# Optimization experiments

Measured on AMD Instinct MI355X. Metric: run time of the kernel, lower is better.

The kernel has to match this reference:

```python
import jax, jax.numpy as jnp
import numpy as np

B, A, T, D, H, K, P = 32, 32, 64, 16, 64, 2, 2
E = A * (A - 1)
TAU = 0.5


def _linear_init(key, fin, fout):
    bound = 1.0 / np.sqrt(fin)
    kw, kb = jax.random.split(key)
    W = jax.random.uniform(kw, (fin, fout), minval=-bound, maxval=bound, dtype=jnp.float32)
    b = jax.random.uniform(kb, (fout,), minval=-bound, maxval=bound, dtype=jnp.float32)
    return W, b


def setup_inputs() -> dict:
    key = jax.random.key(0)
    ks = jax.random.split(key, 12)
    # off-diagonal edge list; rel_rec/rel_send are one-hot [E, A]
    idx = np.array([(i, j) for i in range(A) for j in range(A) if i != j])
    eye = np.eye(A, dtype=np.float32)
    rel_rec = jnp.asarray(eye[idx[:, 0]])
    rel_send = jnp.asarray(eye[idx[:, 1]])
    inputs = jax.random.normal(ks[0], (B, A, T, D), dtype=jnp.float32)
    rel_graph = 0.1 * jax.random.normal(ks[1], (1, 1, E, K), dtype=jnp.float32)
    u = jax.random.uniform(ks[2], (1, 1, E, K), minval=1e-6, maxval=1.0 - 1e-6)
    gumbel = -jnp.log(-jnp.log(u))
    # per-edge-type message MLPs, stacked over K
    w1, b1, w2, b2 = [], [], [], []
    for k in range(K):
        Wa, ba = _linear_init(jax.random.fold_in(ks[3], k), 2 * D, H)
        Wb, bb = _linear_init(jax.random.fold_in(ks[4], k), H, H)
        w1.append(Wa); b1.append(ba); w2.append(Wb); b2.append(bb)
    msg_W1 = jnp.stack(w1); msg_b1 = jnp.stack(b1)
    msg_W2 = jnp.stack(w2); msg_b2 = jnp.stack(b2)
    out_W1, out_b1 = _linear_init(ks[5], D + H, H)
    out_W2, out_b2 = _linear_init(ks[6], H, H)
    out_W3, out_b3 = _linear_init(ks[7], H, D)
    return {"inputs": inputs, "rel_rec": rel_rec, "rel_send": rel_send,
            "rel_graph": rel_graph, "gumbel": gumbel,
            "msg_W1": msg_W1, "msg_b1": msg_b1, "msg_W2": msg_W2, "msg_b2": msg_b2,
            "out_W1": out_W1, "out_b1": out_b1, "out_W2": out_W2, "out_b2": out_b2,
            "out_W3": out_W3, "out_b3": out_b3}


def _single_step(xs, edges, rel_rec, rel_send,
                 msg_W1, msg_b1, msg_W2, msg_b2,
                 out_W1, out_b1, out_W2, out_b2, out_W3, out_b3):
    # xs: [B, Ts, A, D]; gather endpoints -> [B, Ts, E, D]
    recv = jnp.einsum('ea,btad->bted', rel_rec, xs)
    send = jnp.einsum('ea,btad->bted', rel_send, xs)
    pre_msg = jnp.concatenate([send, recv], axis=-1)  # [B,Ts,E,2D]
    all_msgs = jnp.zeros(pre_msg.shape[:-1] + (H,), dtype=xs.dtype)
    for k in range(K):  # small fixed loop over edge types
        m = jax.nn.relu(pre_msg @ msg_W1[k] + msg_b1[k])
        m = jax.nn.relu(m @ msg_W2[k] + msg_b2[k])
        all_msgs = all_msgs + m * edges[..., k:k + 1]
    # scatter-sum messages to receiver nodes: [B,Ts,A,H]
    agg = jnp.einsum('bteh,ea->btah', all_msgs, rel_rec)
    aug = jnp.concatenate([xs, agg], axis=-1)
    p = jax.nn.relu(aug @ out_W1 + out_b1)
    p = jax.nn.relu(p @ out_W2 + out_b2)
    p = p @ out_W3 + out_b3
    return xs + p


def reference(inputs, rel_rec, rel_send, rel_graph, gumbel,
              msg_W1, msg_b1, msg_W2, msg_b2,
              out_W1, out_b1, out_W2, out_b2, out_W3, out_b3):
    # soft gumbel-softmax (hard=False, deterministic via provided noise)
    edges = jax.nn.softmax((rel_graph + gumbel) / TAU, axis=-1)  # [1,1,E,K]
    x = jnp.transpose(inputs, (0, 2, 1, 3))  # [B,T,A,D]
    last = x[:, ::P]  # [B, T/P, A, D]
    preds = []
    for _ in range(P):
        last = _single_step(last, edges, rel_rec, rel_send,
                            msg_W1, msg_b1, msg_W2, msg_b2,
                            out_W1, out_b1, out_W2, out_b2, out_W3, out_b3)
        preds.append(last)
    # interleave: output[:, t*P + i] = preds[i][:, t]
    out = jnp.stack(preds, axis=2).reshape(x.shape[0], -1, A, D)[:, :T - 1]
    return jnp.transpose(out, (0, 2, 1, 3))  # [B, A, T-1, D]
```

## Files before the change

### kernel.cpp

```cpp
#include <hip/hip_runtime.h>

typedef unsigned short u16;
typedef unsigned int u32;
typedef __attribute__((ext_vector_type(8))) short bf16x8;
typedef __attribute__((ext_vector_type(4))) float f32x4;
typedef __attribute__((ext_vector_type(4))) u32 u32x4;

__device__ __forceinline__ u32 cvtpk(float lo, float hi) {
    u32 r; asm("v_cvt_pk_bf16_f32 %0, %1, %2" : "=v"(r) : "v"(lo), "v"(hi)); return r;
}
__device__ __forceinline__ u16 f2bf1(float f) { return (u16)(cvtpk(f, f) & 0xffffu); }

__device__ __forceinline__ u16 f2bf(float f) {
    union { float f; unsigned u; } v; v.f = f;
    unsigned r = (v.u + 0x7FFFu + ((v.u >> 16) & 1u)) >> 16;
    return (u16)r;
}

__global__ void edge_softmax_k(const float* __restrict__ rg,
                               const float* __restrict__ gb,
                               float* __restrict__ ew) {
    int tid = blockIdx.x * 256 + threadIdx.x;
    if (tid >= 1024) return;
    int i = tid >> 5, j = tid & 31;
    float w0 = 0.f, w1 = 0.f;
    if (i != j) {
        int e = i * 31 + j - (j > i ? 1 : 0);
        float a0 = (rg[e * 2 + 0] + gb[e * 2 + 0]) * 2.0f;
        float a1 = (rg[e * 2 + 1] + gb[e * 2 + 1]) * 2.0f;
        float m = fmaxf(a0, a1);
        float e0 = expf(a0 - m), e1 = expf(a1 - m);
        float s = e0 + e1;
        w0 = e0 / s; w1 = e1 / s;
    }
    ew[tid * 2 + 0] = w0;
    ew[tid * 2 + 1] = w1;
}

__global__ void pack_weights_k(const float* __restrict__ W1,
                               const float* __restrict__ W2,
                               const float* __restrict__ OW1,
                               const float* __restrict__ OW2,
                               const float* __restrict__ OW3,
                               u16* __restrict__ wp) {
    int tid = blockIdx.x * 256 + threadIdx.x;
    if (tid < 4096) {
        int j = tid & 7, l = (tid >> 3) & 63, t = (tid >> 9) & 3, k = tid >> 11;
        int kk = 8 * (l >> 4) + j;
        int n  = 32 * (t >> 1) + 8 * ((l & 15) >> 2) + 4 * (t & 1) + (l & 3);
        wp[tid] = f2bf(W1[k * 2048 + kk * 64 + n]);
    } else if (tid < 12288) {
        int x = tid - 4096;
        int j = x & 7, l = (x >> 3) & 63, t = (x >> 9) & 3, s = (x >> 11) & 1, k = x >> 12;
        int kk = 32 * s + 8 * (l >> 4) + j, n = 16 * t + (l & 15);
        wp[tid] = f2bf(W2[k * 4096 + kk * 64 + n]);
    } else if (tid < 18432) {
        int x = tid - 12288;
        int j = x & 7, l = (x >> 3) & 63, t = (x >> 9) & 3, s = x >> 11;
        int kk = 32 * s + 8 * (l >> 4) + j, n = 16 * t + (l & 15);
        wp[tid] = f2bf(kk < 80 ? OW1[kk * 64 + n] : 0.f);
    } else if (tid < 22528) {
        int x = tid - 18432;
        int j = x & 7, l = (x >> 3) & 63, t = (x >> 9) & 3, s = x >> 11;
        int kk = 32 * s + 8 * (l >> 4) + j, n = 16 * t + (l & 15);
        wp[tid] = f2bf(OW2[kk * 64 + n]);
    } else if (tid < 23552) {
        int x = tid - 22528;
        int j = x & 7, l = (x >> 3) & 63, s = x >> 9;
        int kk = 32 * s + 8 * (l >> 4) + j, n = (l & 15);
        wp[tid] = f2bf(OW3[kk * 16 + n]);
    }
}

__global__ __launch_bounds__(256, 2) void nri_decoder_k(
    const float* __restrict__ inputs,
    const float* __restrict__ mb1, const float* __restrict__ mb2,
    const float* __restrict__ ob1, const float* __restrict__ ob2,
    const float* __restrict__ ob3,
    const float* __restrict__ ew,
    const u16*  __restrict__ wp,
    float* __restrict__ out)
{
    __shared__ float xsf[32][16];
    __shared__ __align__(16) u16 xsb[32][24];
    __shared__ __align__(16) float agg2[2][32][68];
    __shared__ __align__(16) u16 augb[32][104];
    __shared__ __align__(16) u16 p1b[32][72];
    __shared__ __align__(16) u16 p2b[32][72];

    const int tid = threadIdx.x;
    const int w = tid >> 6, lane = tid & 63, g = lane >> 4, lr = lane & 15;
    const int kw = w >> 1, w01 = w & 1;
    const int b = blockIdx.x >> 5, tp = blockIdx.x & 31;

    const u16* w1tp = wp;
    const u16* w2p  = wp + 4096;
    const u16* ow1p = wp + 12288;
    const u16* ow2p = wp + 18432;
    const u16* ow3p = wp + 22528;

    for (int idx = tid; idx < 512; idx += 256) {
        int a = idx >> 4, d = idx & 15;
        float v = inputs[(((b * 32 + a) * 64) + 2 * tp) * 16 + d];
        u16 bv = f2bf1(v);
        xsf[a][d] = v;
        xsb[a][d] = bv;
        augb[a][d] = bv;
        augb[a][80 + d] = 0;
    }

    bf16x8 w1t[4], w2f[2][4];
#pragma unroll
    for (int t = 0; t < 4; ++t)
        w1t[t] = *(const bf16x8*)(w1tp + ((kw * 4 + t) * 64 + lane) * 8);
#pragma unroll
    for (int s = 0; s < 2; ++s)
#pragma unroll
        for (int t = 0; t < 4; ++t)
            w2f[s][t] = *(const bf16x8*)(w2p + (((kw * 2 + s) * 4 + t) * 64 + lane) * 8);

    f32x4 b1c[4];
    float b2r[4];
#pragma unroll
    for (int t = 0; t < 4; ++t) {
#pragma unroll
        for (int r = 0; r < 4; ++r)
            b1c[t][r] = mb1[kw * 64 + 32 * (t >> 1) + 8 * g + 4 * (t & 1) + r];
        b2r[t] = mb2[kw * 64 + 16 * t + lr];
    }
    float o1r[4], o2r[4];
#pragma unroll
    for (int t = 0; t < 4; ++t) { o1r[t] = ob1[16 * t + lr]; o2r[t] = ob2[16 * t + lr]; }
    const float o3r = ob3[lr];

    __syncthreads();

    for (int step = 0; step < 2; ++step) {
        for (int p = 0; p < 16; ++p) {
            const int ir = 16 * w01 + p;
            float racc[4] = {0.f, 0.f, 0.f, 0.f};
#pragma unroll
            for (int half = 0; half < 2; ++half) {
                const int m = 2 * ir + half;
                const int e0 = m * 16;
                const int srow = (g < 2) ? (16 * (m & 1) + lr) : (m >> 1);
                const bf16x8 bfrag = *(const bf16x8*)(&xsb[srow][(g & 1) * 8]);

                float ewv[4];
#pragma unroll
                for (int r = 0; r < 4; ++r) ewv[r] = ew[(e0 + 4 * g + r) * 2 + kw];

                f32x4 c0 = __builtin_amdgcn_mfma_f32_16x16x32_bf16(w1t[0], bfrag, b1c[0], 0, 0, 0);
                f32x4 c1 = __builtin_amdgcn_mfma_f32_16x16x32_bf16(w1t[1], bfrag, b1c[1], 0, 0, 0);
                f32x4 c2 = __builtin_amdgcn_mfma_f32_16x16x32_bf16(w1t[2], bfrag, b1c[2], 0, 0, 0);
                f32x4 c3 = __builtin_amdgcn_mfma_f32_16x16x32_bf16(w1t[3], bfrag, b1c[3], 0, 0, 0);

                union { u32 u[8]; bf16x8 v[2]; } a2;
                a2.u[0] = cvtpk(fmaxf(c0[0], 0.f), fmaxf(c0[1], 0.f));
                a2.u[1] = cvtpk(fmaxf(c0[2], 0.f), fmaxf(c0[3], 0.f));
                a2.u[2] = cvtpk(fmaxf(c1[0], 0.f), fmaxf(c1[1], 0.f));
                a2.u[3] = cvtpk(fmaxf(c1[2], 0.f), fmaxf(c1[3], 0.f));
                a2.u[4] = cvtpk(fmaxf(c2[0], 0.f), fmaxf(c2[1], 0.f));
                a2.u[5] = cvtpk(fmaxf(c2[2], 0.f), fmaxf(c2[3], 0.f));
                a2.u[6] = cvtpk(fmaxf(c3[0], 0.f), fmaxf(c3[1], 0.f));
                a2.u[7] = cvtpk(fmaxf(c3[2], 0.f), fmaxf(c3[3], 0.f));

#pragma unroll
                for (int t = 0; t < 4; ++t) {
                    f32x4 d = {b2r[t], b2r[t], b2r[t], b2r[t]};
                    d = __builtin_amdgcn_mfma_f32_16x16x32_bf16(a2.v[0], w2f[0][t], d, 0, 0, 0);
                    d = __builtin_amdgcn_mfma_f32_16x16x32_bf16(a2.v[1], w2f[1][t], d, 0, 0, 0);
#pragma unroll
                    for (int r = 0; r < 4; ++r)
                        racc[t] += fmaxf(d[r], 0.f) * ewv[r];
                }
            }
#pragma unroll
            for (int t = 0; t < 4; ++t) {
                racc[t] += __shfl_xor(racc[t], 16);
                racc[t] += __shfl_xor(racc[t], 32);
            }
            float v = (g & 2) ? ((g & 1) ? racc[3] : racc[2])
                              : ((g & 1) ? racc[1] : racc[0]);
            agg2[kw][ir][16 * g + lr] = v;
        }
        __syncthreads();

        {
            const int a = tid >> 3, cc = (tid & 7) * 8;
            f32x4 x0 = *(const f32x4*)&agg2[0][a][cc];
            f32x4 x1 = *(const f32x4*)&agg2[0][a][cc + 4];
            f32x4 y0 = *(const f32x4*)&agg2[1][a][cc];
            f32x4 y1 = *(const f32x4*)&agg2[1][a][cc + 4];
            x0 += y0; x1 += y1;
            u32x4 q = { cvtpk(x0[0], x0[1]), cvtpk(x0[2], x0[3]),
                        cvtpk(x1[0], x1[1]), cvtpk(x1[2], x1[3]) };
            *(u32x4*)&augb[a][16 + cc] = q;
        }
        __syncthreads();

        {
            f32x4 c0 = {o1r[w], o1r[w], o1r[w], o1r[w]};
            f32x4 c1 = c0;
#pragma unroll
            for (int s = 0; s < 3; ++s) {
                const bf16x8 a0 = *(const bf16x8*)(&augb[lr][32 * s + 8 * g]);
                const bf16x8 a1 = *(const bf16x8*)(&augb[16 + lr][32 * s + 8 * g]);
                const bf16x8 bw = *(const bf16x8*)(ow1p + ((s * 4 + w) * 64 + lane) * 8);
                c0 = __builtin_amdgcn_mfma_f32_16x16x32_bf16(a0, bw, c0, 0, 0, 0);
                c1 = __builtin_amdgcn_mfma_f32_16x16x32_bf16(a1, bw, c1, 0, 0, 0);
            }
#pragma unroll
            for (int r = 0; r < 4; ++r) {
                p1b[4 * g + r][16 * w + lr]      = f2bf1(fmaxf(c0[r], 0.f));
                p1b[16 + 4 * g + r][16 * w + lr] = f2bf1(fmaxf(c1[r], 0.f));
            }
        }
        __syncthreads();

        {
            f32x4 c0 = {o2r[w], o2r[w], o2r[w], o2r[w]};
            f32x4 c1 = c0;
#pragma unroll
            for (int s = 0; s < 2; ++s) {
                const bf16x8 a0 = *(const bf16x8*)(&p1b[lr][32 * s + 8 * g]);
                const bf16x8 a1 = *(const bf16x8*)(&p1b[16 + lr][32 * s + 8 * g]);
                const bf16x8 bw = *(const bf16x8*)(ow2p + ((s * 4 + w) * 64 + lane) * 8);
                c0 = __builtin_amdgcn_mfma_f32_16x16x32_bf16(a0, bw, c0, 0, 0, 0);
                c1 = __builtin_amdgcn_mfma_f32_16x16x32_bf16(a1, bw, c1, 0, 0, 0);
            }
#pragma unroll
            for (int r = 0; r < 4; ++r) {
                p2b[4 * g + r][16 * w + lr]      = f2bf1(fmaxf(c0[r], 0.f));
                p2b[16 + 4 * g + r][16 * w + lr] = f2bf1(fmaxf(c1[r], 0.f));
            }
        }
        __syncthreads();

        if (w < 2) {
            f32x4 c = {o3r, o3r, o3r, o3r};
#pragma unroll
            for (int s = 0; s < 2; ++s) {
                const bf16x8 a0 = *(const bf16x8*)(&p2b[16 * w + lr][32 * s + 8 * g]);
                const bf16x8 bw = *(const bf16x8*)(ow3p + (s * 64 + lane) * 8);
                c = __builtin_amdgcn_mfma_f32_16x16x32_bf16(a0, bw, c, 0, 0, 0);
            }
            const int tt = 2 * tp + step;
#pragma unroll
            for (int r = 0; r < 4; ++r) {
                const int aa = 16 * w + 4 * g + r;
                const float nv = xsf[aa][lr] + c[r];
                u16 bv = f2bf1(nv);
                xsf[aa][lr] = nv;
                xsb[aa][lr] = bv;
                augb[aa][lr] = bv;
                if (tt < 63) out[(((b * 32 + aa) * 63) + tt) * 16 + lr] = nv;
            }
        }
        __syncthreads();
    }
}

extern "C" void kernel_launch(void* const* d_in, const int* in_sizes, int n_in,
                              void* d_out, int out_size, void* d_ws, size_t ws_size,
                              hipStream_t stream) {
    const float* inputs = (const float*)d_in[0];
    const float* rg     = (const float*)d_in[3];
    const float* gb     = (const float*)d_in[4];
    const float* W1     = (const float*)d_in[5];
    const float* mb1    = (const float*)d_in[6];
    const float* W2     = (const float*)d_in[7];
    const float* mb2    = (const float*)d_in[8];
    const float* OW1    = (const float*)d_in[9];
    const float* ob1    = (const float*)d_in[10];
    const float* OW2    = (const float*)d_in[11];
    const float* ob2    = (const float*)d_in[12];
    const float* OW3    = (const float*)d_in[13];
    const float* ob3    = (const float*)d_in[14];

    float* ew = (float*)d_ws;
    u16*   wpk = (u16*)((char*)d_ws + 8192);

    edge_softmax_k<<<4, 256, 0, stream>>>(rg, gb, ew);
    pack_weights_k<<<92, 256, 0, stream>>>(W1, W2, OW1, OW2, OW3, wpk);
    nri_decoder_k<<<1024, 256, 0, stream>>>(inputs, mb1, mb2, ob1, ob2, ob3,
                                            ew, wpk, (float*)d_out);
}
```

Before: 84.46 us.

## Fuse output MLP into register chain using transposed MFMA and LDS-staged weights

```diff
diff --git a/kernel.cpp b/kernel.cpp
--- a/kernel.cpp
+++ b/kernel.cpp
@@ -4,12 +4,12 @@
 typedef unsigned int u32;
 typedef __attribute__((ext_vector_type(8))) short bf16x8;
 typedef __attribute__((ext_vector_type(4))) float f32x4;
+typedef __attribute__((ext_vector_type(2))) u32 u32x2;
 typedef __attribute__((ext_vector_type(4))) u32 u32x4;
 
 __device__ __forceinline__ u32 cvtpk(float lo, float hi) {
     u32 r; asm("v_cvt_pk_bf16_f32 %0, %1, %2" : "=v"(r) : "v"(lo), "v"(hi)); return r;
 }
-__device__ __forceinline__ u16 f2bf1(float f) { return (u16)(cvtpk(f, f) & 0xffffu); }
 
 __device__ __forceinline__ u16 f2bf(float f) {
     union { float f; unsigned u; } v; v.f = f;
@@ -56,19 +56,23 @@
         wp[tid] = f2bf(W2[k * 4096 + kk * 64 + n]);
     } else if (tid < 18432) {
         int x = tid - 12288;
-        int j = x & 7, l = (x >> 3) & 63, t = (x >> 9) & 3, s = x >> 11;
-        int kk = 32 * s + 8 * (l >> 4) + j, n = 16 * t + (l & 15);
-        wp[tid] = f2bf(kk < 80 ? OW1[kk * 64 + n] : 0.f);
+        int j = x & 7, l = (x >> 3) & 63, ts = x >> 9;
+        int s = ts % 3, t = ts / 3;
+        int kk = 32 * s + 8 * (l >> 4) + j;
+        int feat = 32 * (t >> 1) + 8 * ((l & 15) >> 2) + 4 * (t & 1) + (l & 3);
+        wp[tid] = f2bf(kk < 80 ? OW1[kk * 64 + feat] : 0.f);
     } else if (tid < 22528) {
         int x = tid - 18432;
-        int j = x & 7, l = (x >> 3) & 63, t = (x >> 9) & 3, s = x >> 11;
-        int kk = 32 * s + 8 * (l >> 4) + j, n = 16 * t + (l & 15);
-        wp[tid] = f2bf(OW2[kk * 64 + n]);
+        int j = x & 7, l = (x >> 3) & 63, ts = x >> 9;
+        int s = ts & 1, t = ts >> 1;
+        int kk = 32 * s + 8 * (l >> 4) + j;
+        int feat = 32 * (t >> 1) + 8 * ((l & 15) >> 2) + 4 * (t & 1) + (l & 3);
+        wp[tid] = f2bf(OW2[kk * 64 + feat]);
     } else if (tid < 23552) {
         int x = tid - 22528;
         int j = x & 7, l = (x >> 3) & 63, s = x >> 9;
-        int kk = 32 * s + 8 * (l >> 4) + j, n = (l & 15);
-        wp[tid] = f2bf(OW3[kk * 16 + n]);
+        int kk = 32 * s + 8 * (l >> 4) + j;
+        wp[tid] = f2bf(OW3[kk * 16 + (l & 15)]);
     }
 }
 
@@ -81,12 +85,10 @@
     const u16*  __restrict__ wp,
     float* __restrict__ out)
 {
-    __shared__ float xsf[32][16];
-    __shared__ __align__(16) u16 xsb[32][24];
+    __shared__ __align__(16) u16 xsb[2][32][24];
     __shared__ __align__(16) float agg2[2][32][68];
-    __shared__ __align__(16) u16 augb[32][104];
-    __shared__ __align__(16) u16 p1b[32][72];
-    __shared__ __align__(16) u16 p2b[32][72];
+    __shared__ __align__(16) u16 augb[2][32][104];
+    __shared__ __align__(16) u16 owlds[11264];
 
     const int tid = threadIdx.x;
     const int w = tid >> 6, lane = tid & 63, g = lane >> 4, lr = lane & 15;
@@ -95,19 +97,19 @@
 
     const u16* w1tp = wp;
     const u16* w2p  = wp + 4096;
-    const u16* ow1p = wp + 12288;
-    const u16* ow2p = wp + 18432;
-    const u16* ow3p = wp + 22528;
-
-    for (int idx = tid; idx < 512; idx += 256) {
-        int a = idx >> 4, d = idx & 15;
-        float v = inputs[(((b * 32 + a) * 64) + 2 * tp) * 16 + d];
-        u16 bv = f2bf1(v);
-        xsf[a][d] = v;
-        xsb[a][d] = bv;
-        augb[a][d] = bv;
-        augb[a][80 + d] = 0;
-    }
+
+    for (int idx = tid; idx < 1408; idx += 256)
+        *(u32x4*)(&owlds[idx * 8]) = *(const u32x4*)(wp + 12288 + idx * 8);
+
+    if (tid < 128) {
+        const int a = tid >> 2, dd = (tid & 3) * 4;
+        const f32x4 v = *(const f32x4*)(inputs + (((b * 32 + a) * 64) + 2 * tp) * 16 + dd);
+        u32x2 q = { cvtpk(v[0], v[1]), cvtpk(v[2], v[3]) };
+        *(u32x2*)(&xsb[0][a][dd]) = q;
+        *(u32x2*)(&augb[0][a][dd]) = q;
+    }
+    for (int idx = tid; idx < 1024; idx += 256)
+        augb[idx >> 9][(idx >> 4) & 31][80 + (idx & 15)] = 0;
 
     bf16x8 w1t[4], w2f[2][4];
 #pragma unroll
@@ -119,23 +121,31 @@
         for (int t = 0; t < 4; ++t)
             w2f[s][t] = *(const bf16x8*)(w2p + (((kw * 2 + s) * 4 + t) * 64 + lane) * 8);
 
-    f32x4 b1c[4];
+    f32x4 b1c[4], o1c[4], o2c[4], o3c;
     float b2r[4];
 #pragma unroll
     for (int t = 0; t < 4; ++t) {
 #pragma unroll
-        for (int r = 0; r < 4; ++r)
-            b1c[t][r] = mb1[kw * 64 + 32 * (t >> 1) + 8 * g + 4 * (t & 1) + r];
+        for (int r = 0; r < 4; ++r) {
+            const int pi = 32 * (t >> 1) + 8 * g + 4 * (t & 1) + r;
+            b1c[t][r] = mb1[kw * 64 + pi];
+            o1c[t][r] = ob1[pi];
+            o2c[t][r] = ob2[pi];
+        }
         b2r[t] = mb2[kw * 64 + 16 * t + lr];
     }
-    float o1r[4], o2r[4];
-#pragma unroll
-    for (int t = 0; t < 4; ++t) { o1r[t] = ob1[16 * t + lr]; o2r[t] = ob2[16 * t + lr]; }
-    const float o3r = ob3[lr];
+#pragma unroll
+    for (int r = 0; r < 4; ++r) o3c[r] = ob3[4 * g + r];
+
+    const int u = w & 1;
+    const int arow = 16 * u + lr;
+    f32x4 xsreg = *(const f32x4*)(inputs + (((b * 32 + arow) * 64) + 2 * tp) * 16 + 4 * g);
 
     __syncthreads();
 
     for (int step = 0; step < 2; ++step) {
+        const int sp = step & 1;
+
         for (int p = 0; p < 16; ++p) {
             const int ir = 16 * w01 + p;
             float racc[4] = {0.f, 0.f, 0.f, 0.f};
@@ -144,7 +154,7 @@
                 const int m = 2 * ir + half;
                 const int e0 = m * 16;
                 const int srow = (g < 2) ? (16 * (m & 1) + lr) : (m >> 1);
-                const bf16x8 bfrag = *(const bf16x8*)(&xsb[srow][(g & 1) * 8]);
+                const bf16x8 bfrag = *(const bf16x8*)(&xsb[sp][srow][(g & 1) * 8]);
 
                 float ewv[4];
 #pragma unroll
@@ -155,15 +165,15 @@
                 f32x4 c2 = __builtin_amdgcn_mfma_f32_16x16x32_bf16(w1t[2], bfrag, b1c[2], 0, 0, 0);
                 f32x4 c3 = __builtin_amdgcn_mfma_f32_16x16x32_bf16(w1t[3], bfrag, b1c[3], 0, 0, 0);
 
-                union { u32 u[8]; bf16x8 v[2]; } a2;
-                a2.u[0] = cvtpk(fmaxf(c0[0], 0.f), fmaxf(c0[1], 0.f));
-                a2.u[1] = cvtpk(fmaxf(c0[2], 0.f), fmaxf(c0[3], 0.f));
-                a2.u[2] = cvtpk(fmaxf(c1[0], 0.f), fmaxf(c1[1], 0.f));
-                a2.u[3] = cvtpk(fmaxf(c1[2], 0.f), fmaxf(c1[3], 0.f));
-                a2.u[4] = cvtpk(fmaxf(c2[0], 0.f), fmaxf(c2[1], 0.f));
-                a2.u[5] = cvtpk(fmaxf(c2[2], 0.f), fmaxf(c2[3], 0.f));
-                a2.u[6] = cvtpk(fmaxf(c3[0], 0.f), fmaxf(c3[1], 0.f));
-                a2.u[7] = cvtpk(fmaxf(c3[2], 0.f), fmaxf(c3[3], 0.f));
+                union { u32 q[8]; bf16x8 v[2]; } a2;
+                a2.q[0] = cvtpk(fmaxf(c0[0], 0.f), fmaxf(c0[1], 0.f));
+                a2.q[1] = cvtpk(fmaxf(c0[2], 0.f), fmaxf(c0[3], 0.f));
+                a2.q[2] = cvtpk(fmaxf(c1[0], 0.f), fmaxf(c1[1], 0.f));
+                a2.q[3] = cvtpk(fmaxf(c1[2], 0.f), fmaxf(c1[3], 0.f));
+                a2.q[4] = cvtpk(fmaxf(c2[0], 0.f), fmaxf(c2[1], 0.f));
+                a2.q[5] = cvtpk(fmaxf(c2[2], 0.f), fmaxf(c2[3], 0.f));
+                a2.q[6] = cvtpk(fmaxf(c3[0], 0.f), fmaxf(c3[1], 0.f));
+                a2.q[7] = cvtpk(fmaxf(c3[2], 0.f), fmaxf(c3[3], 0.f));
 
 #pragma unroll
                 for (int t = 0; t < 4; ++t) {
@@ -195,66 +205,68 @@
             x0 += y0; x1 += y1;
             u32x4 q = { cvtpk(x0[0], x0[1]), cvtpk(x0[2], x0[3]),
                         cvtpk(x1[0], x1[1]), cvtpk(x1[2], x1[3]) };
-            *(u32x4*)&augb[a][16 + cc] = q;
+            *(u32x4*)&augb[sp][a][16 + cc] = q;
         }
         __syncthreads();
 
         {
-            f32x4 c0 = {o1r[w], o1r[w], o1r[w], o1r[w]};
-            f32x4 c1 = c0;
+            f32x4 c[4] = {o1c[0], o1c[1], o1c[2], o1c[3]};
 #pragma unroll
             for (int s = 0; s < 3; ++s) {
-                const bf16x8 a0 = *(const bf16x8*)(&augb[lr][32 * s + 8 * g]);
-                const bf16x8 a1 = *(const bf16x8*)(&augb[16 + lr][32 * s + 8 * g]);
-                const bf16x8 bw = *(const bf16x8*)(ow1p + ((s * 4 + w) * 64 + lane) * 8);
-                c0 = __builtin_amdgcn_mfma_f32_16x16x32_bf16(a0, bw, c0, 0, 0, 0);
-                c1 = __builtin_amdgcn_mfma_f32_16x16x32_bf16(a1, bw, c1, 0, 0, 0);
-            }
-#pragma unroll
-            for (int r = 0; r < 4; ++r) {
-                p1b[4 * g + r][16 * w + lr]      = f2bf1(fmaxf(c0[r], 0.f));
-                p1b[16 + 4 * g + r][16 * w + lr] = f2bf1(fmaxf(c1[r], 0.f));
-            }
-        }
-        __syncthreads();
-
-        {
-            f32x4 c0 = {o2r[w], o2r[w], o2r[w], o2r[w]};
-            f32x4 c1 = c0;
+                const bf16x8 bB = *(const bf16x8*)(&augb[sp][arow][32 * s + 8 * g]);
+#pragma unroll
+                for (int t = 0; t < 4; ++t) {
+                    const bf16x8 aA = *(const bf16x8*)(&owlds[(t * 3 + s) * 512 + lane * 8]);
+                    c[t] = __builtin_amdgcn_mfma_f32_16x16x32_bf16(aA, bB, c[t], 0, 0, 0);
+                }
+            }
+            union { u32 q[8]; bf16x8 v[2]; } pa;
+            pa.q[0] = cvtpk(fmaxf(c[0][0], 0.f), fmaxf(c[0][1], 0.f));
+            pa.q[1] = cvtpk(fmaxf(c[0][2], 0.f), fmaxf(c[0][3], 0.f));
+            pa.q[2] = cvtpk(fmaxf(c[1][0], 0.f), fmaxf(c[1][1], 0.f));
+            pa.q[3] = cvtpk(fmaxf(c[1][2], 0.f), fmaxf(c[1][3], 0.f));
+            pa.q[4] = cvtpk(fmaxf(c[2][0], 0.f), fmaxf(c[2][1], 0.f));
+            pa.q[5] = cvtpk(fmaxf(c[2][2], 0.f), fmaxf(c[2][3], 0.f));
+            pa.q[6] = cvtpk(fmaxf(c[3][0], 0.f), fmaxf(c[3][1], 0.f));
+            pa.q[7] = cvtpk(fmaxf(c[3][2], 0.f), fmaxf(c[3][3], 0.f));
+
+            f32x4 c2[4] = {o2c[0], o2c[1], o2c[2], o2c[3]};
+#pragma unroll
+            for (int s = 0; s < 2; ++s)
+#pragma unroll
+                for (int t = 0; t < 4; ++t) {
+                    const bf16x8 aA = *(const bf16x8*)(&owlds[6144 + (t * 2 + s) * 512 + lane * 8]);
+                    c2[t] = __builtin_amdgcn_mfma_f32_16x16x32_bf16(aA, pa.v[s], c2[t], 0, 0, 0);
+                }
+            union { u32 q[8]; bf16x8 v[2]; } pb;
+            pb.q[0] = cvtpk(fmaxf(c2[0][0], 0.f), fmaxf(c2[0][1], 0.f));
+            pb.q[1] = cvtpk(fmaxf(c2[0][2], 0.f), fmaxf(c2[0][3], 0.f));
+            pb.q[2] = cvtpk(fmaxf(c2[1][0], 0.f), fmaxf(c2[1][1], 0.f));
+            pb.q[3] = cvtpk(fmaxf(c2[1][2], 0.f), fmaxf(c2[1][3], 0.f));
+            pb.q[4] = cvtpk(fmaxf(c2[2][0], 0.f), fmaxf(c2[2][1], 0.f));
+            pb.q[5] = cvtpk(fmaxf(c2[2][2], 0.f), fmaxf(c2[2][3], 0.f));
+            pb.q[6] = cvtpk(fmaxf(c2[3][0], 0.f), fmaxf(c2[3][1], 0.f));
+            pb.q[7] = cvtpk(fmaxf(c2[3][2], 0.f), fmaxf(c2[3][3], 0.f));
+
+            f32x4 d3 = o3c;
 #pragma unroll
             for (int s = 0; s < 2; ++s) {
-                const bf16x8 a0 = *(const bf16x8*)(&p1b[lr][32 * s + 8 * g]);
-                const bf16x8 a1 = *(const bf16x8*)(&p1b[16 + lr][32 * s + 8 * g]);
-                const bf16x8 bw = *(const bf16x8*)(ow2p + ((s * 4 + w) * 64 + lane) * 8);
-                c0 = __builtin_amdgcn_mfma_f32_16x16x32_bf16(a0, bw, c0, 0, 0, 0);
-                c1 = __builtin_amdgcn_mfma_f32_16x16x32_bf16(a1, bw, c1, 0, 0, 0);
-            }
-#pragma unroll
-            for (int r = 0; r < 4; ++r) {
-                p2b[4 * g + r][16 * w + lr]      = f2bf1(fmaxf(c0[r], 0.f));
-                p2b[16 + 4 * g + r][16 * w + lr] = f2bf1(fmaxf(c1[r], 0.f));
-            }
-        }
-        __syncthreads();
-
-        if (w < 2) {
-            f32x4 c = {o3r, o3r, o3r, o3r};
-#pragma unroll
-            for (int s = 0; s < 2; ++s) {
-                const bf16x8 a0 = *(const bf16x8*)(&p2b[16 * w + lr][32 * s + 8 * g]);
-                const bf16x8 bw = *(const bf16x8*)(ow3p + (s * 64 + lane) * 8);
-                c = __builtin_amdgcn_mfma_f32_16x16x32_bf16(a0, bw, c, 0, 0, 0);
-            }
-            const int tt = 2 * tp + step;
-#pragma unroll
-            for (int r = 0; r < 4; ++r) {
-                const int aa = 16 * w + 4 * g + r;
-                const float nv = xsf[aa][lr] + c[r];
-                u16 bv = f2bf1(nv);
-                xsf[aa][lr] = nv;
-                xsb[aa][lr] = bv;
-                augb[aa][lr] = bv;
-                if (tt < 63) out[(((b * 32 + aa) * 63) + tt) * 16 + lr] = nv;
+                const bf16x8 aA = *(const bf16x8*)(&owlds[10240 + s * 512 + lane * 8]);
+                d3 = __builtin_amdgcn_mfma_f32_16x16x32_bf16(aA, pb.v[s], d3, 0, 0, 0);
+            }
+
+            const f32x4 nv = xsreg + d3;
+            xsreg = nv;
+            const u32 q0 = cvtpk(nv[0], nv[1]);
+            const u32 q1 = cvtpk(nv[2], nv[3]);
+            if (w < 2) {
+                u32x2 qq = {q0, q1};
+                *(u32x2*)(&xsb[sp ^ 1][arow][4 * g]) = qq;
+                *(u32x2*)(&augb[sp ^ 1][arow][4 * g]) = qq;
+            } else {
+                const int tt = 2 * tp + step;
+                if (tt < 63)
+                    *(f32x4*)(out + (((b * 32 + arow) * 63) + tt) * 16 + 4 * g) = nv;
             }
         }
         __syncthreads();
```

Measured after the change: 82.46 us (median of 2 runs). 1.02x faster.
